# Performance work log

Measured on AMD Instinct MI355X. Metric: run time of the kernel, lower is better.

## Reference

```python
import jax, jax.numpy as jnp
import numpy as np

B, L, D, H = 2, 2048, 1024, 16
DK = D // H


def setup_inputs() -> dict:
    key = jax.random.key(0)
    ks = jax.random.split(key, 12)
    s = 1.0 / np.sqrt(D)
    return {
        "x": jax.random.normal(ks[0], (B, L, D), jnp.float32),
        "timestamps": jnp.sort(jax.random.uniform(ks[1], (B, L), jnp.float32) * 1000.0, axis=-1),
        "decay_values": jax.random.normal(ks[2], (B, L), jnp.float32),
        "pad_mask": jnp.ones((B, L), dtype=bool),
        "Wq": jax.random.normal(ks[3], (D, D), jnp.float32) * s,
        "bq": jnp.zeros((D,), jnp.float32),
        "Wk": jax.random.normal(ks[4], (D, D), jnp.float32) * s,
        "bk": jnp.zeros((D,), jnp.float32),
        "Wv": jax.random.normal(ks[5], (D, D), jnp.float32) * s,
        "bv": jnp.zeros((D,), jnp.float32),
        "Wo": jax.random.normal(ks[6], (D, D), jnp.float32) * s,
        "bo": jnp.zeros((D,), jnp.float32),
        "lam": jnp.float32(0.01),
    }


def reference(x, timestamps, decay_values, pad_mask, Wq, bq, Wk, bk, Wv, bv, Wo, bo, lam):
    b, l, d = x.shape
    # projections (torch Linear: x @ W.T + b), split heads -> [B,H,L,DK]
    def split_heads(y):
        return y.reshape(b, l, H, DK).transpose(0, 2, 1, 3)
    Q = split_heads(x @ Wq.T + bq)
    K = split_heads(x @ Wk.T + bk)
    V = split_heads(x @ Wv.T + bv)

    scores = jnp.einsum("bhqd,bhkd->bhqk", Q, K) / np.sqrt(DK)
    # temporal log-decay bias
    t_diff = jnp.abs(timestamps[:, :, None] - timestamps[:, None, :])  # [B,L,L]
    denom = jax.lax.stop_gradient(jnp.maximum(t_diff.max(), 1.0))  # matches .item() constant
    scores = scores - jnp.abs(lam) * jnp.log1p(t_diff / denom)[:, None, :, :]

    causal = jnp.triu(jnp.ones((l, l), dtype=bool), k=1)  # True above diag -> masked
    neg_inf = jnp.float32(-jnp.inf)
    scores = jnp.where(causal[None, None], neg_inf, scores)
    scores = jnp.where(pad_mask[:, None, None, :], scores, neg_inf)

    attn = jnp.nan_to_num(jax.nn.softmax(scores, axis=-1), nan=0.0)
    out = jnp.einsum("bhqk,bhkd->bhqd", attn, V)
    out = out.transpose(0, 2, 1, 3).reshape(b, l, d)
    return out @ Wo.T + bo
```

## Files before the change

### kernel.cpp

```cpp
#include <hip/hip_runtime.h>
#include <hip/hip_bf16.h>
#include <math.h>

#define Bsz 2
#define Lsz 2048
#define Dsz 1024
#define Hsz 16
#define DKsz 64
#define NW_ELEMS (1u << 20)

typedef __attribute__((ext_vector_type(8))) short short8;
typedef __attribute__((ext_vector_type(4))) short short4v;
typedef __attribute__((ext_vector_type(4))) float v4f;
typedef unsigned short ushortT;
#define MFMA16(a, b, c) __builtin_amdgcn_mfma_f32_16x16x32_bf16(a, b, c, 0, 0, 0)
#define LOG2E 1.44269504088896340736f

union V8 { short8 v8; short4v v4[2]; };
union A8 { short8 v8; unsigned w[4]; };

__device__ __forceinline__ ushortT f2bf(float f) {
    union { float f; unsigned u; } x; x.f = f;
    unsigned r = x.u + 0x7fffu + ((x.u >> 16) & 1u);
    return (ushortT)(r >> 16);
}
__device__ __forceinline__ void glds16(const void* g, void* l) {
    __builtin_amdgcn_global_load_lds(
        (const __attribute__((address_space(1))) void*)g,
        (__attribute__((address_space(3))) void*)l, 16, 0, 0);
}

__global__ __launch_bounds__(256) void cast_denom(const float* __restrict__ x,
                                                  const float* __restrict__ Wq,
                                                  const float* __restrict__ Wk,
                                                  const float* __restrict__ Wv,
                                                  const float* __restrict__ Wo,
                                                  const float* __restrict__ t,
                                                  const float* __restrict__ bq,
                                                  const float* __restrict__ bk,
                                                  const float* __restrict__ bv,
                                                  ushortT* __restrict__ xb,
                                                  ushortT* __restrict__ Wqkvb,
                                                  ushortT* __restrict__ Wob,
                                                  float* __restrict__ denom_out,
                                                  float* __restrict__ cbias,
                                                  int ncast) {
    const int NX = Bsz * Lsz * Dsz;
    int tid = threadIdx.x;
    if ((int)blockIdx.x == ncast) {
        __shared__ float smx[256], smn[256];
        for (int i = tid; i < 3 * Dsz; i += 256)
            cbias[i] = (i < Dsz) ? bq[i] : (i < 2 * Dsz ? bk[i - Dsz] : bv[i - 2 * Dsz]);
        float best = 1.0f;
        for (int b = 0; b < Bsz; ++b) {
            float mx = -INFINITY, mn = INFINITY;
            for (int i = tid; i < Lsz; i += 256) {
                float v = t[b * Lsz + i];
                mx = fmaxf(mx, v);
                mn = fminf(mn, v);
            }
            smx[tid] = mx; smn[tid] = mn;
            __syncthreads();
            for (int s = 128; s > 0; s >>= 1) {
                if (tid < s) {
                    smx[tid] = fmaxf(smx[tid], smx[tid + s]);
                    smn[tid] = fminf(smn[tid], smn[tid + s]);
                }
                __syncthreads();
            }
            best = fmaxf(best, smx[0] - smn[0]);
            __syncthreads();
        }
        if (tid == 0) denom_out[0] = best;
        return;
    }
    int i = (blockIdx.x * 256 + tid) * 4;
    const float* src; ushortT* dst;
    if (i < NX) { src = x + i; dst = xb + i; }
    else {
        int j = i - NX;
        if (j < 3 * (int)NW_ELEMS) {
            int w = j >> 20, o = j & (NW_ELEMS - 1);
            src = (w == 0 ? Wq : (w == 1 ? Wk : Wv)) + o;
            dst = Wqkvb + j;
        } else {
            int o = j - 3 * NW_ELEMS;
            src = Wo + o; dst = Wob + o;
        }
    }
    float4 v = *(const float4*)src;
    ushort4 o4;
    o4.x = f2bf(v.x); o4.y = f2bf(v.y); o4.z = f2bf(v.z); o4.w = f2bf(v.w);
    *(ushort4*)dst = o4;
}

template <bool QKV, int MT, int NT, int WMW, int WNW, int PERX>
__global__ __launch_bounds__(256) void gemm_mfma(const ushortT* __restrict__ A,
                                                 const ushortT* __restrict__ W,
                                                 const float* __restrict__ bias,
                                                 void* __restrict__ O0,
                                                 void* __restrict__ O1,
                                                 void* __restrict__ O2) {
    const int K = Dsz;
    constexpr int MROWS = MT / WMW, NCOLS = NT / WNW;
    constexpr int MTI = MROWS / 16, NTI = NCOLS / 16;
    __shared__ ushortT As[2 * MT * 32];
    __shared__ ushortT Ws[2 * NT * 32];
    int tid = threadIdx.x;
    int wid = tid >> 6, lane = tid & 63, quad = lane >> 4, m16 = lane & 15;
    int wm = wid / WNW, wn = wid % WNW;
    int id = blockIdx.x;
    int xcd = id & 7, r = id >> 3;
    int n0 = (xcd * PERX + r % PERX) * NT;
    int m0 = (r / PERX) * MT;
    int lrow = lane >> 2;
    int lcol = ((lane & 3) ^ (lrow & 3)) * 8;
    int rchunk = (quad ^ (m16 & 3)) * 8;

    v4f acc[MTI][NTI];
#pragma unroll
    for (int i = 0; i < MTI; ++i)
#pragma unroll
        for (int j = 0; j < NTI; ++j) acc[i][j] = (v4f){0.f, 0.f, 0.f, 0.f};

    for (int kt = 0; kt < K; kt += 64) {
        __syncthreads();
#pragma unroll
        for (int p = 0; p < 2; ++p) {
            int kp = kt + p * 32 + lcol;
#pragma unroll
            for (int i = 0; i < MT / 64; ++i) {
                int r0 = wid * (MT / 4) + i * 16;
                glds16(A + (size_t)(m0 + r0 + lrow) * K + kp, &As[p * MT * 32 + r0 * 32]);
            }
#pragma unroll
            for (int i = 0; i < NT / 64; ++i) {
                int r0 = wid * (NT / 4) + i * 16;
                glds16(W + (size_t)(n0 + r0 + lrow) * K + kp, &Ws[p * NT * 32 + r0 * 32]);
            }
        }
        __syncthreads();
#pragma unroll
        for (int p = 0; p < 2; ++p) {
            short8 af[MTI], wf[NTI];
#pragma unroll
            for (int mt = 0; mt < MTI; ++mt)
                af[mt] = *(const short8*)&As[p * MT * 32 +
                                            (wm * MROWS + mt * 16 + m16) * 32 + rchunk];
#pragma unroll
            for (int nt = 0; nt < NTI; ++nt)
                wf[nt] = *(const short8*)&Ws[p * NT * 32 +
                                            (wn * NCOLS + nt * 16 + m16) * 32 + rchunk];
#pragma unroll
            for (int mt = 0; mt < MTI; ++mt)
#pragma unroll
                for (int nt = 0; nt < NTI; ++nt)
                    acc[mt][nt] = MFMA16(af[mt], wf[nt], acc[mt][nt]);
        }
    }

    if (QKV) {
        int region = n0 >> 10;
        float scale = (region == 0) ? 0.125f * LOG2E : 1.0f;
#pragma unroll
        for (int nt = 0; nt < NTI; ++nt) {
            int col = n0 + wn * NCOLS + nt * 16 + m16;
            float bv_ = bias[col];
            int c1 = col & (Dsz - 1);
#pragma unroll
            for (int mt = 0; mt < MTI; ++mt) {
                int row0 = m0 + wm * MROWS + mt * 16 + quad * 4;
                if (region == 2) {
                    ushort4 pk;
                    pk.x = f2bf(acc[mt][nt][0] + bv_);
                    pk.y = f2bf(acc[mt][nt][1] + bv_);
                    pk.z = f2bf(acc[mt][nt][2] + bv_);
                    pk.w = f2bf(acc[mt][nt][3] + bv_);
                    int bb = row0 >> 11, seq = row0 & (Lsz - 1);
                    *(ushort4*)&((ushortT*)O2)[((size_t)bb * Dsz + c1) * Lsz + seq] = pk;
                } else {
                    ushortT* dst = (ushortT*)(region == 0 ? O0 : O1);
#pragma unroll
                    for (int rr = 0; rr < 4; ++rr)
                        dst[(size_t)(row0 + rr) * Dsz + c1] =
                            f2bf((acc[mt][nt][rr] + bv_) * scale);
                }
            }
        }
    } else {
#pragma unroll
        for (int nt = 0; nt < NTI; ++nt) {
            int col = n0 + wn * NCOLS + nt * 16 + m16;
            float bv_ = bias[col];
#pragma unroll
            for (int mt = 0; mt < MTI; ++mt) {
                int row0 = m0 + wm * MROWS + mt * 16 + quad * 4;
#pragma unroll
                for (int rr = 0; rr < 4; ++rr)
                    ((float*)O0)[(size_t)(row0 + rr) * Dsz + col] = acc[mt][nt][rr] + bv_;
            }
        }
    }
}

#define STAGE(JT, BUF)                                                         \
  {                                                                            \
    size_t ko = (size_t)(JT) * 64 * Dsz;                                       \
    int vo = (JT) * 64;                                                        \
    glds16(kst + ko, &Ks[BUF][(wid * 16) * 64]);                               \
    glds16(kst + ko + 8 * (size_t)Dsz, &Ks[BUF][(wid * 16 + 8) * 64]);         \
    glds16(vst + vo, &Vs[BUF][(wid * 16) * 64]);                               \
    glds16(vst + vo + 8 * (size_t)Lsz, &Vs[BUF][(wid * 16 + 8) * 64]);         \
    if (tid < 64) Tsl[BUF][tid] = ts[bL + (JT) * 64 + tid];                    \
  }

#define ATTN_TILE(CB, DIAG)                                                    \
  {                                                                            \
    const ushortT* Kc = &Ks[CB][0];                                            \
    const ushortT* Vc = &Vs[CB][0];                                            \
    unsigned pw[8];                                                            \
    _Pragma("unroll")                                                          \
    for (int ct = 0; ct < 4; ++ct) {                                           \
      bool need = !(DIAG) || (ct <= wid);                                      \
      if (need) {                                                              \
        const char* kr = (const char*)(Kc + (ct * 16 + m16) * 64);             \
        short8 kf0 = *(const short8*)(kr + koff0);                             \
        short8 kf1 = *(const short8*)(kr + koff1);                             \
        v4f tk4 = *(const v4f*)&Tsl[CB][ct * 16 + quad * 4];                   \
        v4f sv = (v4f){0.f, 0.f, 0.f, 0.f};                                    \
        sv = MFMA16(kf0, qf0, sv);                                             \
        sv = MFMA16(kf1, qf1, sv);                                             \
        unsigned pu[4];                                                        \
        _Pragma("unroll")                                                      \
        for (int rr = 0; rr < 4; ++rr) {                                       \
          float w = dtq - tk4[rr];                                             \
          float wf = (float)__builtin_bit_cast(int, w);                        \
          float f = fmaf(na23, wf, sv[rr]);                                    \
          if ((DIAG) && ct == wid)                                             \
            f = (quad * 4 + rr <= m16) ? f : -INFINITY;                        \
          float pv = __builtin_amdgcn_exp2f(f);                                \
          unsigned u = __builtin_bit_cast(unsigned, pv);                       \
          lac[rr] += __builtin_bit_cast(float, u & 0xffff0000u);               \
          pu[rr] = u;                                                          \
        }                                                                      \
        pw[2 * ct]     = __builtin_amdgcn_perm(pu[1], pu[0], 0x07060302u);     \
        pw[2 * ct + 1] = __builtin_amdgcn_perm(pu[3], pu[2], 0x07060302u);     \
      } else {                                                                 \
        pw[2 * ct] = 0u; pw[2 * ct + 1] = 0u;                                  \
      }                                                                        \
    }                                                                          \
    A8 af0, af1;                                                               \
    af0.w[0] = pw[0]; af0.w[1] = pw[1]; af0.w[2] = pw[2]; af0.w[3] = pw[3];    \
    af1.w[0] = pw[4]; af1.w[1] = pw[5]; af1.w[2] = pw[6]; af1.w[3] = pw[7];    \
    bool hi = !(DIAG) || (wid >= 2);                                           \
    _Pragma("unroll")                                                          \
    for (int dt = 0; dt < 4; ++dt) {                                           \
      const char* vr = (const char*)(Vc + (dt * 16 + m16) * 64) + h8;          \
      V8 u0;                                                                   \
      u0.v4[0] = *(const short4v*)(vr + ((vs0 ^ 0) << 4));                     \
      u0.v4[1] = *(const short4v*)(vr + ((vs0 ^ 2) << 4));                     \
      o[dt] = MFMA16(af0.v8, u0.v8, o[dt]);                                    \
      if (hi) {                                                                \
        V8 u1;                                                                 \
        u1.v4[0] = *(const short4v*)(vr + ((vs0 ^ 4) << 4));                   \
        u1.v4[1] = *(const short4v*)(vr + ((vs0 ^ 6) << 4));                   \
        o[dt] = MFMA16(af1.v8, u1.v8, o[dt]);                                  \
      }                                                                        \
    }                                                                          \
  }

__global__ __launch_bounds__(256, 4) void attn_mfma(const ushortT* __restrict__ Qb,
                                                    const ushortT* __restrict__ Kb,
                                                    const ushortT* __restrict__ Vtg,
                                                    const float* __restrict__ ts,
                                                    const float* __restrict__ denomp,
                                                    const float* __restrict__ lamp,
                                                    ushortT* __restrict__ AOb) {
    int id = blockIdx.x;
    int xcd = id & 7, cu = (id >> 3) & 31, j = id >> 8;
    int bh = xcd * 4 + (cu >> 3);
    int b = bh >> 4, h = bh & 15;
    int p = ((cu & 7) << 1) | (j >> 1);
    int qt = (j & 1) ? (31 - p) : p;

    int tid = threadIdx.x;
    int wid = tid >> 6, lane = tid & 63, quad = lane >> 4, m16 = lane & 15;
    int sw = m16 & 7;

    __shared__ ushortT Ks[2][64 * 64];
    __shared__ ushortT Vs[2][64 * 64];
    __shared__ float Tsl[2][64];

    const size_t bL = (size_t)b * Lsz;
    float denom = denomp[0];
    float alam = fabsf(lamp[0]);
    float na23 = -alam * (1.0f / 8388608.0f);

    int qbase = qt * 64 + wid * 16;
    float dtq = denom + ts[bL + qbase + m16];

    const ushortT* qptr = Qb + (bL + qbase + m16) * (size_t)Dsz + h * 64 + quad * 8;
    short8 qf0 = *(const short8*)qptr;
    short8 qf1 = *(const short8*)(qptr + 32);

    int srow = lane >> 3;
    int sslot = (lane & 7) ^ srow;
    const ushortT* kst = Kb + (bL + wid * 16 + srow) * (size_t)Dsz + h * 64 + sslot * 8;
    const ushortT* vst = Vtg + ((size_t)b * Dsz + h * 64 + wid * 16 + srow) * Lsz + sslot * 8;

    int koff0 = (quad ^ sw) << 4;
    int koff1 = ((quad | 4) ^ sw) << 4;
    int vs0 = (quad >> 1) ^ sw;
    int h8 = (quad & 1) * 8;

    v4f o[4];
    float lac[4];
#pragma unroll
    for (int i = 0; i < 4; ++i) { o[i] = (v4f){0.f, 0.f, 0.f, 0.f}; lac[i] = 0.f; }

    STAGE(0, 0)
    __syncthreads();
    for (int jt = 0; jt < qt; ++jt) {
        int cb = jt & 1;
        STAGE(jt + 1, cb ^ 1)
        ATTN_TILE(cb, false)
        __syncthreads();
    }
    {
        int cb = qt & 1;
        ATTN_TILE(cb, true)
    }

    float lacc = (lac[0] + lac[1]) + (lac[2] + lac[3]);
    float l1 = lacc + __shfl_xor(lacc, 16);
    float lf = l1 + __shfl_xor(l1, 32);

    ushortT* obase = AOb + (bL + qbase) * (size_t)Dsz + h * 64 + m16;
#pragma unroll
    for (int rr = 0; rr < 4; ++rr) {
        float lr = __shfl(lf, quad * 4 + rr, 16);
        float invl = 1.0f / lr;
        int qrow = quad * 4 + rr;
#pragma unroll
        for (int dt = 0; dt < 4; ++dt)
            obase[(size_t)qrow * Dsz + dt * 16] = f2bf(o[dt][rr] * invl);
    }
}

extern "C" void kernel_launch(void* const* d_in, const int* in_sizes, int n_in,
                              void* d_out, int out_size, void* d_ws, size_t ws_size,
                              hipStream_t stream) {
    const float* x   = (const float*)d_in[0];
    const float* ts  = (const float*)d_in[1];
    const float* Wq  = (const float*)d_in[4];
    const float* bq  = (const float*)d_in[5];
    const float* Wk  = (const float*)d_in[6];
    const float* bk  = (const float*)d_in[7];
    const float* Wv  = (const float*)d_in[8];
    const float* bv  = (const float*)d_in[9];
    const float* Wo  = (const float*)d_in[10];
    const float* bo  = (const float*)d_in[11];
    const float* lam = (const float*)d_in[12];

    const size_t NX = (size_t)Bsz * Lsz * Dsz;
    const size_t NW = (size_t)NW_ELEMS;

    char* w = (char*)d_ws;
    float* denom = (float*)w;            w += 256;
    float* cbias = (float*)w;            w += 3 * Dsz * 4 + 256;
    ushortT* xb    = (ushortT*)w;        w += NX * 2;
    ushortT* Wqkvb = (ushortT*)w;        w += 3 * NW * 2;
    ushortT* Wob   = (ushortT*)w;        w += NW * 2;
    ushortT* Qb    = (ushortT*)w;        w += NX * 2;
    ushortT* Kbf   = (ushortT*)w;        w += NX * 2;
    ushortT* Vtg   = (ushortT*)w;        w += NX * 2;
    ushortT* AOb   = (ushortT*)w;        w += NX * 2;

    int ncast = (int)((NX + 4 * NW) / 4 / 256);
    cast_denom<<<ncast + 1, 256, 0, stream>>>(x, Wq, Wk, Wv, Wo, ts, bq, bk, bv,
                                              xb, Wqkvb, Wob, denom, cbias, ncast);

    gemm_mfma<true, 64, 128, 1, 4, 3><<<1536, 256, 0, stream>>>(
        xb, Wqkvb, cbias, Qb, Kbf, Vtg);

    attn_mfma<<<1024, 256, 0, stream>>>(Qb, Kbf, Vtg, ts, denom, lam, AOb);

    gemm_mfma<false, 64, 64, 2, 2, 2><<<1024, 256, 0, stream>>>(
        AOb, Wob, bo, d_out, nullptr, nullptr);
}
```

Baseline: 207.0 us.

## Use 128-row query tiles with 8 waves per attention block sharing K/V staging

The attention kernel now launches 512 blocks of 512 threads, each covering 128 query rows with 8 waves. Every staged 64-key K/V tile is reused by twice as many queries, which halves global-to-LDS traffic per query. The last diagonal tile is split in two, with waves 4-7 handling a second tile after a sync. Key timestamps are now read straight from global memory instead of being staged in LDS. The trade-off is a coarser causal tail that wastes more work in the diagonal tiles, and fewer, larger blocks that may change occupancy and load balance.

```diff
diff --git a/kernel.cpp b/kernel.cpp
--- a/kernel.cpp
+++ b/kernel.cpp
@@ -207,26 +207,23 @@
   {                                                                            \
     size_t ko = (size_t)(JT) * 64 * Dsz;                                       \
     int vo = (JT) * 64;                                                        \
-    glds16(kst + ko, &Ks[BUF][(wid * 16) * 64]);                               \
-    glds16(kst + ko + 8 * (size_t)Dsz, &Ks[BUF][(wid * 16 + 8) * 64]);         \
-    glds16(vst + vo, &Vs[BUF][(wid * 16) * 64]);                               \
-    glds16(vst + vo + 8 * (size_t)Lsz, &Vs[BUF][(wid * 16 + 8) * 64]);         \
-    if (tid < 64) Tsl[BUF][tid] = ts[bL + (JT) * 64 + tid];                    \
+    glds16(kst + ko, &Ks[BUF][(wid * 8) * 64]);                                \
+    glds16(vst + vo, &Vs[BUF][(wid * 8) * 64]);                                \
   }
 
-#define ATTN_TILE(CB, DIAG)                                                    \
+#define ATTN_TILE(CB, K0, DW)                                                  \
   {                                                                            \
     const ushortT* Kc = &Ks[CB][0];                                            \
     const ushortT* Vc = &Vs[CB][0];                                            \
+    const float* tsk = tsb + (K0);                                             \
     unsigned pw[8];                                                            \
     _Pragma("unroll")                                                          \
     for (int ct = 0; ct < 4; ++ct) {                                           \
-      bool need = !(DIAG) || (ct <= wid);                                      \
-      if (need) {                                                              \
+      if (ct <= (DW)) {                                                        \
         const char* kr = (const char*)(Kc + (ct * 16 + m16) * 64);             \
         short8 kf0 = *(const short8*)(kr + koff0);                             \
         short8 kf1 = *(const short8*)(kr + koff1);                             \
-        v4f tk4 = *(const v4f*)&Tsl[CB][ct * 16 + quad * 4];                   \
+        v4f tk4 = *(const v4f*)(tsk + ct * 16);                                \
         v4f sv = (v4f){0.f, 0.f, 0.f, 0.f};                                    \
         sv = MFMA16(kf0, qf0, sv);                                             \
         sv = MFMA16(kf1, qf1, sv);                                             \
@@ -236,8 +233,7 @@
           float w = dtq - tk4[rr];                                             \
           float wf = (float)__builtin_bit_cast(int, w);                        \
           float f = fmaf(na23, wf, sv[rr]);                                    \
-          if ((DIAG) && ct == wid)                                             \
-            f = (quad * 4 + rr <= m16) ? f : -INFINITY;                        \
+          if (ct == (DW)) f = (quad * 4 + rr <= m16) ? f : -INFINITY;          \
           float pv = __builtin_amdgcn_exp2f(f);                                \
           unsigned u = __builtin_bit_cast(unsigned, pv);                       \
           lac[rr] += __builtin_bit_cast(float, u & 0xffff0000u);               \
@@ -252,7 +248,7 @@
     A8 af0, af1;                                                               \
     af0.w[0] = pw[0]; af0.w[1] = pw[1]; af0.w[2] = pw[2]; af0.w[3] = pw[3];    \
     af1.w[0] = pw[4]; af1.w[1] = pw[5]; af1.w[2] = pw[6]; af1.w[3] = pw[7];    \
-    bool hi = !(DIAG) || (wid >= 2);                                           \
+    bool hi = (DW) >= 2;                                                       \
     _Pragma("unroll")                                                          \
     for (int dt = 0; dt < 4; ++dt) {                                           \
       const char* vr = (const char*)(Vc + (dt * 16 + m16) * 64) + h8;          \
@@ -269,7 +265,7 @@
     }                                                                          \
   }
 
-__global__ __launch_bounds__(256, 4) void attn_mfma(const ushortT* __restrict__ Qb,
+__global__ __launch_bounds__(512, 4) void attn_mfma(const ushortT* __restrict__ Qb,
                                                     const ushortT* __restrict__ Kb,
                                                     const ushortT* __restrict__ Vtg,
                                                     const float* __restrict__ ts,
@@ -280,8 +276,8 @@
     int xcd = id & 7, cu = (id >> 3) & 31, j = id >> 8;
     int bh = xcd * 4 + (cu >> 3);
     int b = bh >> 4, h = bh & 15;
-    int p = ((cu & 7) << 1) | (j >> 1);
-    int qt = (j & 1) ? (31 - p) : p;
+    int pc = cu & 7;
+    int s = j ? (15 - pc) : pc;
 
     int tid = threadIdx.x;
     int wid = tid >> 6, lane = tid & 63, quad = lane >> 4, m16 = lane & 15;
@@ -289,15 +285,15 @@
 
     __shared__ ushortT Ks[2][64 * 64];
     __shared__ ushortT Vs[2][64 * 64];
-    __shared__ float Tsl[2][64];
 
     const size_t bL = (size_t)b * Lsz;
     float denom = denomp[0];
     float alam = fabsf(lamp[0]);
     float na23 = -alam * (1.0f / 8388608.0f);
 
-    int qbase = qt * 64 + wid * 16;
+    int qbase = s * 128 + wid * 16;
     float dtq = denom + ts[bL + qbase + m16];
+    const float* tsb = ts + bL + quad * 4;
 
     const ushortT* qptr = Qb + (bL + qbase + m16) * (size_t)Dsz + h * 64 + quad * 8;
     short8 qf0 = *(const short8*)qptr;
@@ -305,8 +301,8 @@
 
     int srow = lane >> 3;
     int sslot = (lane & 7) ^ srow;
-    const ushortT* kst = Kb + (bL + wid * 16 + srow) * (size_t)Dsz + h * 64 + sslot * 8;
-    const ushortT* vst = Vtg + ((size_t)b * Dsz + h * 64 + wid * 16 + srow) * Lsz + sslot * 8;
+    const ushortT* kst = Kb + (bL + wid * 8 + srow) * (size_t)Dsz + h * 64 + sslot * 8;
+    const ushortT* vst = Vtg + ((size_t)b * Dsz + h * 64 + wid * 8 + srow) * Lsz + sslot * 8;
 
     int koff0 = (quad ^ sw) << 4;
     int koff1 = ((quad | 4) ^ sw) << 4;
@@ -320,15 +316,21 @@
 
     STAGE(0, 0)
     __syncthreads();
-    for (int jt = 0; jt < qt; ++jt) {
+    int nfull = 2 * s;
+    for (int jt = 0; jt < nfull; ++jt) {
         int cb = jt & 1;
         STAGE(jt + 1, cb ^ 1)
-        ATTN_TILE(cb, false)
+        ATTN_TILE(cb, jt * 64, 4)
         __syncthreads();
     }
     {
-        int cb = qt & 1;
-        ATTN_TILE(cb, true)
+        STAGE(nfull + 1, 1)
+        int dw = (wid < 4) ? wid : 4;
+        ATTN_TILE(0, nfull * 64, dw)
+        __syncthreads();
+    }
+    if (wid >= 4) {
+        ATTN_TILE(1, (nfull + 1) * 64, wid - 4)
     }
 
     float lacc = (lac[0] + lac[1]) + (lac[2] + lac[3]);
@@ -383,7 +385,7 @@
     gemm_mfma<true, 64, 128, 1, 4, 3><<<1536, 256, 0, stream>>>(
         xb, Wqkvb, cbias, Qb, Kbf, Vtg);
 
-    attn_mfma<<<1024, 256, 0, stream>>>(Qb, Kbf, Vtg, ts, denom, lam, AOb);
+    attn_mfma<<<512, 512, 0, stream>>>(Qb, Kbf, Vtg, ts, denom, lam, AOb);
 
     gemm_mfma<false, 64, 64, 2, 2, 2><<<1024, 256, 0, stream>>>(
         AOb, Wob, bo, d_out, nullptr, nullptr);
```

After: 216.4 us. +4.6%, slower.

## Load V fragments directly into registers and unroll attention loop by two

Applied to the files above, without the earlier changes.

V tiles are no longer staged through LDS. Each lane now prefetches its V fragments from global memory straight into registers one tile ahead, using two register sets (vA/vB) with the main loop unrolled by two. Timestamps are staged with an async global-to-LDS load, and MFMA sections get raised wave priority via s_setprio. This cuts LDS traffic and capacity use, at the cost of 32 extra short4 registers per lane and narrower, strided global loads for V, which may hurt coalescing and occupancy.

```diff
diff --git a/kernel.cpp b/kernel.cpp
--- a/kernel.cpp
+++ b/kernel.cpp
@@ -28,6 +28,11 @@
     __builtin_amdgcn_global_load_lds(
         (const __attribute__((address_space(1))) void*)g,
         (__attribute__((address_space(3))) void*)l, 16, 0, 0);
+}
+__device__ __forceinline__ void glds4(const void* g, void* l) {
+    __builtin_amdgcn_global_load_lds(
+        (const __attribute__((address_space(1))) void*)g,
+        (__attribute__((address_space(3))) void*)l, 4, 0, 0);
 }
 
 __global__ __launch_bounds__(256) void cast_denom(const float* __restrict__ x,
@@ -203,30 +208,35 @@
     }
 }
 
-#define STAGE(JT, BUF)                                                         \
+#define STAGEK(JT, BUF)                                                        \
   {                                                                            \
     size_t ko = (size_t)(JT) * 64 * Dsz;                                       \
-    int vo = (JT) * 64;                                                        \
     glds16(kst + ko, &Ks[BUF][(wid * 16) * 64]);                               \
     glds16(kst + ko + 8 * (size_t)Dsz, &Ks[BUF][(wid * 16 + 8) * 64]);         \
-    glds16(vst + vo, &Vs[BUF][(wid * 16) * 64]);                               \
-    glds16(vst + vo + 8 * (size_t)Lsz, &Vs[BUF][(wid * 16 + 8) * 64]);         \
-    if (tid < 64) Tsl[BUF][tid] = ts[bL + (JT) * 64 + tid];                    \
+    if (tid < 64) glds4(tsg + (JT) * 64 + tid, &Tsf[BUF][0]);                  \
   }
 
-#define ATTN_TILE(CB, DIAG)                                                    \
+#define PREFV(VV, K0)                                                          \
+  _Pragma("unroll")                                                            \
+  for (int dt = 0; dt < 4; ++dt) {                                             \
+    const ushortT* vp = vbase + (size_t)(dt * 16) * Lsz + (K0);                \
+    VV[dt * 4 + 0] = *(const short4v*)vp;                                      \
+    VV[dt * 4 + 1] = *(const short4v*)(vp + 16);                               \
+    VV[dt * 4 + 2] = *(const short4v*)(vp + 32);                               \
+    VV[dt * 4 + 3] = *(const short4v*)(vp + 48);                               \
+  }
+
+#define ATTN_TILE(CB, DW, VV)                                                  \
   {                                                                            \
     const ushortT* Kc = &Ks[CB][0];                                            \
-    const ushortT* Vc = &Vs[CB][0];                                            \
     unsigned pw[8];                                                            \
     _Pragma("unroll")                                                          \
     for (int ct = 0; ct < 4; ++ct) {                                           \
-      bool need = !(DIAG) || (ct <= wid);                                      \
-      if (need) {                                                              \
+      if (ct <= (DW)) {                                                        \
         const char* kr = (const char*)(Kc + (ct * 16 + m16) * 64);             \
         short8 kf0 = *(const short8*)(kr + koff0);                             \
         short8 kf1 = *(const short8*)(kr + koff1);                             \
-        v4f tk4 = *(const v4f*)&Tsl[CB][ct * 16 + quad * 4];                   \
+        v4f tk4 = *(const v4f*)&Tsf[CB][ct * 16 + quad * 4];                   \
         v4f sv = (v4f){0.f, 0.f, 0.f, 0.f};                                    \
         sv = MFMA16(kf0, qf0, sv);                                             \
         sv = MFMA16(kf1, qf1, sv);                                             \
@@ -236,8 +246,7 @@
           float w = dtq - tk4[rr];                                             \
           float wf = (float)__builtin_bit_cast(int, w);                        \
           float f = fmaf(na23, wf, sv[rr]);                                    \
-          if ((DIAG) && ct == wid)                                             \
-            f = (quad * 4 + rr <= m16) ? f : -INFINITY;                        \
+          if (ct == (DW)) f = (quad * 4 + rr <= m16) ? f : -INFINITY;          \
           float pv = __builtin_amdgcn_exp2f(f);                                \
           unsigned u = __builtin_bit_cast(unsigned, pv);                       \
           lac[rr] += __builtin_bit_cast(float, u & 0xffff0000u);               \
@@ -252,21 +261,22 @@
     A8 af0, af1;                                                               \
     af0.w[0] = pw[0]; af0.w[1] = pw[1]; af0.w[2] = pw[2]; af0.w[3] = pw[3];    \
     af1.w[0] = pw[4]; af1.w[1] = pw[5]; af1.w[2] = pw[6]; af1.w[3] = pw[7];    \
-    bool hi = !(DIAG) || (wid >= 2);                                           \
+    bool hi = (DW) >= 2;                                                       \
+    __builtin_amdgcn_s_setprio(1);                                             \
     _Pragma("unroll")                                                          \
     for (int dt = 0; dt < 4; ++dt) {                                           \
-      const char* vr = (const char*)(Vc + (dt * 16 + m16) * 64) + h8;          \
       V8 u0;                                                                   \
-      u0.v4[0] = *(const short4v*)(vr + ((vs0 ^ 0) << 4));                     \
-      u0.v4[1] = *(const short4v*)(vr + ((vs0 ^ 2) << 4));                     \
+      u0.v4[0] = VV[dt * 4 + 0];                                               \
+      u0.v4[1] = VV[dt * 4 + 1];                                               \
       o[dt] = MFMA16(af0.v8, u0.v8, o[dt]);                                    \
       if (hi) {                                                                \
         V8 u1;                                                                 \
-        u1.v4[0] = *(const short4v*)(vr + ((vs0 ^ 4) << 4));                   \
-        u1.v4[1] = *(const short4v*)(vr + ((vs0 ^ 6) << 4));                   \
+        u1.v4[0] = VV[dt * 4 + 2];                                             \
+        u1.v4[1] = VV[dt * 4 + 3];                                             \
         o[dt] = MFMA16(af1.v8, u1.v8, o[dt]);                                  \
       }                                                                        \
     }                                                                          \
+    __builtin_amdgcn_s_setprio(0);                                             \
   }
 
 __global__ __launch_bounds__(256, 4) void attn_mfma(const ushortT* __restrict__ Qb,
@@ -288,8 +298,7 @@
     int sw = m16 & 7;
 
     __shared__ ushortT Ks[2][64 * 64];
-    __shared__ ushortT Vs[2][64 * 64];
-    __shared__ float Tsl[2][64];
+    __shared__ float Tsf[2][64];
 
     const size_t bL = (size_t)b * Lsz;
     float denom = denomp[0];
@@ -298,6 +307,7 @@
 
     int qbase = qt * 64 + wid * 16;
     float dtq = denom + ts[bL + qbase + m16];
+    const float* tsg = ts + bL;
 
     const ushortT* qptr = Qb + (bL + qbase + m16) * (size_t)Dsz + h * 64 + quad * 8;
     short8 qf0 = *(const short8*)qptr;
@@ -306,29 +316,39 @@
     int srow = lane >> 3;
     int sslot = (lane & 7) ^ srow;
     const ushortT* kst = Kb + (bL + wid * 16 + srow) * (size_t)Dsz + h * 64 + sslot * 8;
-    const ushortT* vst = Vtg + ((size_t)b * Dsz + h * 64 + wid * 16 + srow) * Lsz + sslot * 8;
+    const ushortT* vbase = Vtg + ((size_t)b * Dsz + h * 64 + m16) * Lsz + quad * 4;
 
     int koff0 = (quad ^ sw) << 4;
     int koff1 = ((quad | 4) ^ sw) << 4;
-    int vs0 = (quad >> 1) ^ sw;
-    int h8 = (quad & 1) * 8;
 
     v4f o[4];
     float lac[4];
+    short4v vA[16], vB[16];
 #pragma unroll
     for (int i = 0; i < 4; ++i) { o[i] = (v4f){0.f, 0.f, 0.f, 0.f}; lac[i] = 0.f; }
 
-    STAGE(0, 0)
+    STAGEK(0, 0)
+    PREFV(vA, 0)
     __syncthreads();
-    for (int jt = 0; jt < qt; ++jt) {
-        int cb = jt & 1;
-        STAGE(jt + 1, cb ^ 1)
-        ATTN_TILE(cb, false)
+    int jt = 0;
+    for (; jt + 2 <= qt; jt += 2) {
+        STAGEK(jt + 1, 1)
+        PREFV(vB, (jt + 1) * 64)
+        ATTN_TILE(0, 4, vA)
         __syncthreads();
-    }
-    {
-        int cb = qt & 1;
-        ATTN_TILE(cb, true)
+        STAGEK(jt + 2, 0)
+        PREFV(vA, (jt + 2) * 64)
+        ATTN_TILE(1, 4, vB)
+        __syncthreads();
+    }
+    if (jt < qt) {
+        STAGEK(qt, 1)
+        PREFV(vB, qt * 64)
+        ATTN_TILE(0, 4, vA)
+        __syncthreads();
+        ATTN_TILE(1, wid, vB)
+    } else {
+        ATTN_TILE(0, wid, vA)
     }
 
     float lacc = (lac[0] + lac[1]) + (lac[2] + lac[3]);
```

After: 341.1 us. +64.8%, slower.
